# Kernel tuning notes

Measured on AMD Instinct MI355X. Metric: run time of the kernel, lower is better.

The kernel has to match this reference:

```python
import jax, jax.numpy as jnp
import numpy as np

N_NODES = 50000
N_EDGES = 800000
N_GRAPHS = 500
F_NODE = 64
C = 64          # out_channels
F_EDGE = 16     # num_edge_features (== hidden_channels of edge MLP)
N_CLASSES = 2
L = 2           # n_hidden_layers
N_BLOCKS = 6
N_HCONV = N_BLOCKS * L  # 12 hidden PDNConvs
EPS = 1e-5


def setup_inputs() -> dict:
    key = jax.random.key(0)
    ks = jax.random.split(key, 24)

    def w(k, shape, fan_in):
        return (jax.random.normal(k, shape, jnp.float32) / np.sqrt(fan_in)).astype(jnp.float32)

    x = jax.random.normal(ks[0], (N_NODES, F_NODE), jnp.float32)
    src = jax.random.randint(ks[1], (N_EDGES,), 0, N_NODES, dtype=jnp.int32)
    dst = jax.random.randint(ks[2], (N_EDGES,), 0, N_NODES, dtype=jnp.int32)
    edge_index = jnp.stack([src, dst])
    # graph assignment covering all N_GRAPHS segments
    batch = ((jnp.arange(N_NODES) * N_GRAPHS) // N_NODES).astype(jnp.int32)
    edge_attr = jax.random.uniform(ks[3], (N_EDGES, F_EDGE), jnp.float32)

    inp = dict(x=x, edge_index=edge_index, batch=batch, dropout=0, edge_attr=edge_attr)
    # conv1 params
    inp["Wlin1"] = w(ks[4], (F_NODE, C), F_NODE)
    inp["bias1"] = jnp.zeros((C,), jnp.float32)
    inp["m1W1"] = w(ks[5], (F_EDGE, F_EDGE), F_EDGE)
    inp["m1b1"] = jnp.zeros((F_EDGE,), jnp.float32)
    inp["m2W1"] = w(ks[6], (F_EDGE, 1), F_EDGE)
    inp["m2b1"] = jnp.zeros((1,), jnp.float32)
    # 12 stacked hidden PDNConv params
    inp["hWlin"] = w(ks[7], (N_HCONV, C, C), C)
    inp["hbias"] = jnp.zeros((N_HCONV, C), jnp.float32)
    inp["hm1W"] = w(ks[8], (N_HCONV, F_EDGE, F_EDGE), F_EDGE)
    inp["hm1b"] = jnp.zeros((N_HCONV, F_EDGE), jnp.float32)
    inp["hm2W"] = w(ks[9], (N_HCONV, F_EDGE, 1), F_EDGE)
    inp["hm2b"] = jnp.zeros((N_HCONV, 1), jnp.float32)
    # readout linear
    inp["linW"] = w(ks[10], (C, N_CLASSES), C)
    inp["linb"] = jnp.zeros((N_CLASSES,), jnp.float32)
    return inp


def pdn_conv(x, edge_attr, src, dst, mW1, mb1, mW2, mb2, Wlin, bias):
    """PyG PDNConv: edge MLP -> sigmoid edge weight, self-loops, gcn_norm, weighted sum aggregation."""
    n = x.shape[0]
    ew = jax.nn.sigmoid(jax.nn.relu(edge_attr @ mW1 + mb1) @ mW2 + mb2)[:, 0]  # [E]
    loop = jnp.arange(n, dtype=src.dtype)
    s = jnp.concatenate([src, loop])
    d = jnp.concatenate([dst, loop])
    wf = jnp.concatenate([ew, jnp.ones((n,), ew.dtype)])  # self-loop weight = 1
    deg = jax.ops.segment_sum(wf, d, num_segments=n)
    dis = jnp.where(deg > 0, jax.lax.rsqrt(jnp.maximum(deg, 1e-12)), 0.0)
    norm = dis[s] * wf * dis[d]                      # [E+N]
    h = x @ Wlin                                     # [N, C]
    out = jax.ops.segment_sum(h[s] * norm[:, None], d, num_segments=n)
    return out + bias


def bn_relu(x):
    # fresh BatchNorm in training mode: batch stats, weight=1, bias=0 (biased variance)
    mu = x.mean(0)
    var = x.var(0)
    return jax.nn.relu((x - mu) * jax.lax.rsqrt(var + EPS))


def reference(x, edge_index, batch, dropout, edge_attr,
              Wlin1, bias1, m1W1, m1b1, m2W1, m2b1,
              hWlin, hbias, hm1W, hm1b, hm2W, hm2b, linW, linb):
    src, dst = edge_index[0], edge_index[1]
    cur = pdn_conv(x, edge_attr, src, dst, m1W1, m1b1, m2W1, m2b1, Wlin1, bias1)
    xs = [cur]  # dense additive skips: x0, x1, ...
    for b in range(N_BLOCKS):
        for i in range(L):
            j = b * L + i
            cur = pdn_conv(bn_relu(cur), edge_attr, src, dst,
                           hm1W[j], hm1b[j], hm2W[j], hm2b[j], hWlin[j], hbias[j])
        cur = cur + sum(xs)
        xs.append(cur)
    x6 = jax.nn.relu(cur)
    pooled = jax.ops.segment_max(x6, batch, num_segments=N_GRAPHS)  # global max pool
    # dropout is a no-op in eval mode
    return pooled @ linW + linb
```

## Files before the change

### kernel.cpp

```cpp
#include <hip/hip_runtime.h>
#include <math.h>

#define NN 50000
#define NE 800000
#define NG 500
#define NCONV 13
#define WSTRIDE 304
#define SCAN_B 196
#define NBN 12
#define BNP_REPS 64

__device__ __forceinline__ float bl(unsigned u) { return __uint_as_float(u << 16); }
__device__ __forceinline__ float bh(unsigned u) { return __uint_as_float(u & 0xFFFF0000u); }
__device__ __forceinline__ unsigned f2b(float f) {
    unsigned u = __float_as_uint(f);
    return (u + 0x7FFFu + ((u >> 16) & 1u)) >> 16;
}


__global__ void zero_init_k(int* __restrict__ cursor, float* __restrict__ bnpart,
                            const float* __restrict__ m1W1, const float* __restrict__ m1b1,
                            const float* __restrict__ m2W1, const float* __restrict__ m2b1,
                            const float* __restrict__ hm1W, const float* __restrict__ hm1b,
                            const float* __restrict__ hm2W, const float* __restrict__ hm2b,
                            float* __restrict__ wbuf) {
    int i = blockIdx.x * 256 + threadIdx.x;
    if (i < NN) cursor[i] = 0;
    if (i < NBN * BNP_REPS * 128) bnpart[i] = 0.f;
    if (i < NCONV * 289) {
        int cc = i / 289, r = i % 289;
        float v;
        if (r < 256)      v = cc ? hm1W[(cc - 1) * 256 + r] : m1W1[r];
        else if (r < 272) v = cc ? hm1b[(cc - 1) * 16 + (r - 256)] : m1b1[r - 256];
        else if (r < 288) v = cc ? hm2W[(cc - 1) * 16 + (r - 272)] : m2W1[r - 272];
        else              v = cc ? hm2b[cc - 1] : m2b1[0];
        wbuf[cc * WSTRIDE + r] = v;
    }
}


__global__ void count_k(const int* __restrict__ dstp, int* __restrict__ cnt) {
    int e = blockIdx.x * 256 + threadIdx.x;
    if (e >= NE) return;
    atomicAdd(cnt + dstp[e], 1);
}

__global__ __launch_bounds__(256) void scan_blocksum_k(const int* __restrict__ cnt, int* __restrict__ bsum) {
    int i = blockIdx.x * 256 + threadIdx.x;
    int v = (i < NN) ? cnt[i] : 0;
    __shared__ int red[256];
    red[threadIdx.x] = v;
    __syncthreads();
    for (int off = 128; off > 0; off >>= 1) {
        if (threadIdx.x < off) red[threadIdx.x] += red[threadIdx.x + off];
        __syncthreads();
    }
    if (threadIdx.x == 0) bsum[blockIdx.x] = red[0];
}

__global__ __launch_bounds__(256) void scan_bsum_k(int* __restrict__ bsum, int* __restrict__ row_start) {
    __shared__ int ss[256];
    int t = threadIdx.x;
    int v = (t < SCAN_B) ? bsum[t] : 0;
    ss[t] = v;
    __syncthreads();
    for (int off = 1; off < 256; off <<= 1) {
        int add = (t >= off) ? ss[t - off] : 0;
        __syncthreads();
        ss[t] += add;
        __syncthreads();
    }
    if (t < SCAN_B) bsum[t] = (t == 0) ? 0 : ss[t - 1];
    if (t == 0) row_start[NN] = NE;
}

__global__ __launch_bounds__(256) void scan_local_k(int* __restrict__ cnt_cursor, const int* __restrict__ bsum,
                                                    int* __restrict__ row_start) {
    __shared__ int ss[256];
    int i = blockIdx.x * 256 + threadIdx.x;
    int t = threadIdx.x;
    int v = (i < NN) ? cnt_cursor[i] : 0;
    ss[t] = v;
    __syncthreads();
    for (int off = 1; off < 256; off <<= 1) {
        int add = (t >= off) ? ss[t - off] : 0;
        __syncthreads();
        ss[t] += add;
        __syncthreads();
    }
    int excl = bsum[blockIdx.x] + ((t == 0) ? 0 : ss[t - 1]);
    if (i < NN) {
        row_start[i] = excl;
        cnt_cursor[i] = excl;
    }
}

__global__ void scatter_k(const int* __restrict__ srcp, const int* __restrict__ dstp,
                          int* __restrict__ cursor, int* __restrict__ csr_src, int* __restrict__ csr_eid) {
    int e = blockIdx.x * 256 + threadIdx.x;
    if (e >= NE) return;
    int p = atomicAdd(cursor + dstp[e], 1);
    csr_src[p] = srcp[e];
    csr_eid[p] = e;
}


__global__ __launch_bounds__(256, 4) void edge_mlp_k(const float* __restrict__ attr, const int* __restrict__ eid_arr,
                                                     const float* __restrict__ wbuf, float* __restrict__ ew) {
    int k = blockIdx.x * 256 + threadIdx.x;
    if (k >= NE) return;
    int eid = eid_arr[k];
    const float4* a4 = (const float4*)(attr + (size_t)eid * 16);
    float4 A0 = a4[0], A1 = a4[1], A2 = a4[2], A3 = a4[3];
    float a[16] = {A0.x, A0.y, A0.z, A0.w, A1.x, A1.y, A1.z, A1.w,
                   A2.x, A2.y, A2.z, A2.w, A3.x, A3.y, A3.z, A3.w};
    for (int cc = 0; cc < NCONV; cc++) {
        const float* wb = wbuf + cc * WSTRIDE;
        float hb[16];
        #pragma unroll
        for (int o = 0; o < 16; o++) hb[o] = wb[256 + o];
        #pragma unroll
        for (int i = 0; i < 16; i++) {
            float av = a[i];
            #pragma unroll
            for (int o = 0; o < 16; o++) hb[o] = fmaf(av, wb[i * 16 + o], hb[o]);
        }
        float z = wb[288];
        #pragma unroll
        for (int o = 0; o < 16; o++) {
            float hv = hb[o] > 0.f ? hb[o] : 0.f;
            z = fmaf(hv, wb[272 + o], z);
        }
        ew[(size_t)cc * NE + k] = 1.f / (1.f + __expf(-z));
    }
}

__global__ void deg_dis_k(const int* __restrict__ row_start, const float* __restrict__ ew,
                          float* __restrict__ dis) {
    int n = blockIdx.x * 256 + threadIdx.x;
    int cc = blockIdx.y;
    if (n >= NN) return;
    int s0 = row_start[n], s1 = row_start[n + 1];
    const float* e = ew + (size_t)cc * NE;
    float s = 1.f;
    for (int k = s0; k < s1; k++) s += e[k];
    dis[cc * NN + n] = rsqrtf(s);
}


template <bool BN>
__global__ __launch_bounds__(256, 4) void gemm_k(const void* __restrict__ Xv, const float* __restrict__ Wg,
                                                 const float* __restrict__ bnpart, const float* __restrict__ disv,
                                                 unsigned short* __restrict__ Hs) {
    __shared__ float bsum[128];
    __shared__ float mus[64];
    __shared__ float invs[64];
    int t = threadIdx.x;
    if (BN) {
        if (t < 128) {
            float s = 0.f;
            for (int rp = 0; rp < BNP_REPS; rp++) s += bnpart[rp * 128 + t];
            bsum[t] = s;
        }
        __syncthreads();
        if (t < 64) {
            float mu = bsum[t] * (1.f / NN);
            float var = bsum[64 + t] * (1.f / NN) - mu * mu;
            var = var < 0.f ? 0.f : var;
            mus[t] = mu;
            invs[t] = rsqrtf(var + 1e-5f);
        }
        __syncthreads();
    }
    int l = t & 63;
    int colb = __builtin_amdgcn_readfirstlane((t >> 6) * 16);
    int row = blockIdx.x * 64 + l;
    if (row >= NN) return;
    float acc[16];
    #pragma unroll
    for (int c = 0; c < 16; c++) acc[c] = 0.f;
    const float* wcol = Wg + colb;
    if (BN) {
        const uint4* x4 = (const uint4*)((const unsigned short*)Xv + (size_t)row * 64);
        for (int kq = 0; kq < 8; kq++) {
            uint4 uv = x4[kq];
            float xs[8] = {bl(uv.x), bh(uv.x), bl(uv.y), bh(uv.y),
                           bl(uv.z), bh(uv.z), bl(uv.w), bh(uv.w)};
            #pragma unroll
            for (int j = 0; j < 8; j++) {
                int k = kq * 8 + j;
                float v = (xs[j] - mus[k]) * invs[k];
                v = v > 0.f ? v : 0.f;
                const float* wr = wcol + k * 64;
                #pragma unroll
                for (int c = 0; c < 16; c++) acc[c] = fmaf(v, wr[c], acc[c]);
            }
        }
    } else {
        const float4* x4 = (const float4*)((const float*)Xv + (size_t)row * 64);
        for (int kq = 0; kq < 16; kq++) {
            float4 xv = x4[kq];
            float xs[4] = {xv.x, xv.y, xv.z, xv.w};
            #pragma unroll
            for (int j = 0; j < 4; j++) {
                int k = kq * 4 + j;
                float v = xs[j];
                const float* wr = wcol + k * 64;
                #pragma unroll
                for (int c = 0; c < 16; c++) acc[c] = fmaf(v, wr[c], acc[c]);
            }
        }
    }
    float dsc = disv[row];
    unsigned out[8];
    #pragma unroll
    for (int q = 0; q < 8; q++) {
        out[q] = f2b(acc[2 * q] * dsc) | (f2b(acc[2 * q + 1] * dsc) << 16);
    }
    uint4* o4 = (uint4*)(Hs + (size_t)row * 64 + colb);
    uint4 t0; t0.x = out[0]; t0.y = out[1]; t0.z = out[2]; t0.w = out[3];
    uint4 t1; t1.x = out[4]; t1.y = out[5]; t1.z = out[6]; t1.w = out[7];
    o4[0] = t0;
    o4[1] = t1;
}


template <int MODE, int STATS>
__global__ __launch_bounds__(256) void aggregate_k(const unsigned short* __restrict__ Hs, const int* __restrict__ row_start,
                                                   const int* __restrict__ csr_src, const float* __restrict__ w,
                                                   const float* __restrict__ dis, const float* __restrict__ bias,
                                                   unsigned short* __restrict__ curb16, float* __restrict__ S,
                                                   float* __restrict__ finalv, float* __restrict__ bnpart) {
    int t = threadIdx.x;
    int wvid = t >> 6;
    int lane = t & 63;
    int g = lane >> 3;
    int li = lane & 7;
    int node = blockIdx.x * 32 + wvid * 8 + g;
    bool valid = node < NN;
    int s0 = 0, s1 = 0;
    if (valid) { s0 = row_start[node]; s1 = row_start[node + 1]; }
    int fb = li * 8;
    size_t oi = (size_t)node * 64 + fb;
    float dn = 0.f;
    uint4 us = {0, 0, 0, 0};
    float4 b0 = {0, 0, 0, 0}, b1 = {0, 0, 0, 0};
    float4 sa = {0, 0, 0, 0}, sb = {0, 0, 0, 0};
    if (valid) {
        dn = dis[node];
        us = *(const uint4*)(Hs + (size_t)node * 64 + fb);
        b0 = *(const float4*)(bias + fb);
        b1 = *(const float4*)(bias + fb + 4);
        if (MODE >= 2) {
            sa = *(const float4*)(S + oi);
            sb = *(const float4*)(S + oi + 4);
        }
    }
    float acc[8];
    #pragma unroll
    for (int j = 0; j < 8; j++) acc[j] = 0.f;
    int k = s0;
    for (; k + 4 <= s1; k += 4) {
        int i0 = csr_src[k], i1 = csr_src[k + 1], i2 = csr_src[k + 2], i3 = csr_src[k + 3];
        float w0 = w[k], w1 = w[k + 1], w2 = w[k + 2], w3 = w[k + 3];
        uint4 u0 = *(const uint4*)(Hs + (size_t)i0 * 64 + fb);
        uint4 u1 = *(const uint4*)(Hs + (size_t)i1 * 64 + fb);
        uint4 u2 = *(const uint4*)(Hs + (size_t)i2 * 64 + fb);
        uint4 u3 = *(const uint4*)(Hs + (size_t)i3 * 64 + fb);
        acc[0] = fmaf(bl(u0.x), w0, acc[0]); acc[1] = fmaf(bh(u0.x), w0, acc[1]);
        acc[2] = fmaf(bl(u0.y), w0, acc[2]); acc[3] = fmaf(bh(u0.y), w0, acc[3]);
        acc[4] = fmaf(bl(u0.z), w0, acc[4]); acc[5] = fmaf(bh(u0.z), w0, acc[5]);
        acc[6] = fmaf(bl(u0.w), w0, acc[6]); acc[7] = fmaf(bh(u0.w), w0, acc[7]);
        acc[0] = fmaf(bl(u1.x), w1, acc[0]); acc[1] = fmaf(bh(u1.x), w1, acc[1]);
        acc[2] = fmaf(bl(u1.y), w1, acc[2]); acc[3] = fmaf(bh(u1.y), w1, acc[3]);
        acc[4] = fmaf(bl(u1.z), w1, acc[4]); acc[5] = fmaf(bh(u1.z), w1, acc[5]);
        acc[6] = fmaf(bl(u1.w), w1, acc[6]); acc[7] = fmaf(bh(u1.w), w1, acc[7]);
        acc[0] = fmaf(bl(u2.x), w2, acc[0]); acc[1] = fmaf(bh(u2.x), w2, acc[1]);
        acc[2] = fmaf(bl(u2.y), w2, acc[2]); acc[3] = fmaf(bh(u2.y), w2, acc[3]);
        acc[4] = fmaf(bl(u2.z), w2, acc[4]); acc[5] = fmaf(bh(u2.z), w2, acc[5]);
        acc[6] = fmaf(bl(u2.w), w2, acc[6]); acc[7] = fmaf(bh(u2.w), w2, acc[7]);
        acc[0] = fmaf(bl(u3.x), w3, acc[0]); acc[1] = fmaf(bh(u3.x), w3, acc[1]);
        acc[2] = fmaf(bl(u3.y), w3, acc[2]); acc[3] = fmaf(bh(u3.y), w3, acc[3]);
        acc[4] = fmaf(bl(u3.z), w3, acc[4]); acc[5] = fmaf(bh(u3.z), w3, acc[5]);
        acc[6] = fmaf(bl(u3.w), w3, acc[6]); acc[7] = fmaf(bh(u3.w), w3, acc[7]);
    }
    for (; k < s1; k++) {
        int ia = csr_src[k];
        float wa = w[k];
        uint4 ua = *(const uint4*)(Hs + (size_t)ia * 64 + fb);
        acc[0] = fmaf(bl(ua.x), wa, acc[0]); acc[1] = fmaf(bh(ua.x), wa, acc[1]);
        acc[2] = fmaf(bl(ua.y), wa, acc[2]); acc[3] = fmaf(bh(ua.y), wa, acc[3]);
        acc[4] = fmaf(bl(ua.z), wa, acc[4]); acc[5] = fmaf(bh(ua.z), wa, acc[5]);
        acc[6] = fmaf(bl(ua.w), wa, acc[6]); acc[7] = fmaf(bh(ua.w), wa, acc[7]);
    }
    float vv[8];
    #pragma unroll
    for (int j = 0; j < 8; j++) vv[j] = 0.f;
    if (valid) {
        float hs[8] = {bl(us.x), bh(us.x), bl(us.y), bh(us.y), bl(us.z), bh(us.z), bl(us.w), bh(us.w)};
        float bb[8] = {b0.x, b0.y, b0.z, b0.w, b1.x, b1.y, b1.z, b1.w};
        #pragma unroll
        for (int j = 0; j < 8; j++) vv[j] = fmaf(dn, acc[j] + hs[j], bb[j]);
        if (MODE >= 2) {
            float ss[8] = {sa.x, sa.y, sa.z, sa.w, sb.x, sb.y, sb.z, sb.w};
            #pragma unroll
            for (int j = 0; j < 8; j++) vv[j] += ss[j];
            if (MODE == 2) {
                *(float4*)(S + oi) = make_float4(ss[0] + vv[0], ss[1] + vv[1], ss[2] + vv[2], ss[3] + vv[3]);
                *(float4*)(S + oi + 4) = make_float4(ss[4] + vv[4], ss[5] + vv[5], ss[6] + vv[6], ss[7] + vv[7]);
            }
        }
        if (MODE == 1) {
            *(float4*)(S + oi) = make_float4(vv[0], vv[1], vv[2], vv[3]);
            *(float4*)(S + oi + 4) = make_float4(vv[4], vv[5], vv[6], vv[7]);
        }
        if (MODE == 3) {
            *(float4*)(finalv + oi) = make_float4(vv[0], vv[1], vv[2], vv[3]);
            *(float4*)(finalv + oi + 4) = make_float4(vv[4], vv[5], vv[6], vv[7]);
        } else {
            uint4 ob;
            ob.x = f2b(vv[0]) | (f2b(vv[1]) << 16);
            ob.y = f2b(vv[2]) | (f2b(vv[3]) << 16);
            ob.z = f2b(vv[4]) | (f2b(vv[5]) << 16);
            ob.w = f2b(vv[6]) | (f2b(vv[7]) << 16);
            *(uint4*)(curb16 + oi) = ob;
        }
    }
    if (STATS) {
        __shared__ float reds[32 * 65];
        __shared__ float redq[32 * 65];
        int gg = wvid * 8 + g;
        #pragma unroll
        for (int j = 0; j < 8; j++) {
            float v = valid ? vv[j] : 0.f;
            reds[gg * 65 + fb + j] = v;
            redq[gg * 65 + fb + j] = v * v;
        }
        __syncthreads();
        if (t < 128) {
            int f = t & 63;
            const float* src = (t < 64) ? reds : redq;
            float s = 0.f;
            #pragma unroll
            for (int i = 0; i < 32; i++) s += src[i * 65 + f];
            int rep = blockIdx.x & (BNP_REPS - 1);
            atomicAdd(bnpart + rep * 128 + ((t < 64) ? 0 : 64) + f, s);
        }
    }
}


__global__ __launch_bounds__(256) void pool_final_k(const float* __restrict__ cur, const float* __restrict__ linW,
                                                    const float* __restrict__ linb, float* __restrict__ outp) {
    int gph = blockIdx.x;
    int c = threadIdx.x & 63, rq = threadIdx.x >> 6;
    int r0 = gph * 100;
    float m = 0.f;
    for (int r = r0 + rq; r < r0 + 100; r += 4) {
        float v = cur[(size_t)r * 64 + c];
        m = v > m ? v : m;
    }
    __shared__ float red[256];
    red[threadIdx.x] = m;
    __syncthreads();
    if (rq == 0) {
        float a = red[c], b = red[64 + c], d = red[128 + c], e = red[192 + c];
        a = a > b ? a : b;
        d = d > e ? d : e;
        a = a > d ? a : d;
        float p0 = a * linW[c * 2 + 0];
        float p1 = a * linW[c * 2 + 1];
        #pragma unroll
        for (int off = 32; off > 0; off >>= 1) {
            p0 += __shfl_down(p0, off, 64);
            p1 += __shfl_down(p1, off, 64);
        }
        if (c == 0) {
            outp[gph * 2 + 0] = p0 + linb[0];
            outp[gph * 2 + 1] = p1 + linb[1];
        }
    }
}


extern "C" void kernel_launch(void* const* d_in, const int* in_sizes, int n_in,
                              void* d_out, int out_size, void* d_ws, size_t ws_size,
                              hipStream_t stream) {
    const float* x        = (const float*)d_in[0];
    const int*   ei       = (const int*)d_in[1];
    const int*   srcp     = ei;
    const int*   dstp     = ei + NE;
    const float* edge_attr= (const float*)d_in[4];
    const float* Wlin1    = (const float*)d_in[5];
    const float* bias1    = (const float*)d_in[6];
    const float* m1W1     = (const float*)d_in[7];
    const float* m1b1     = (const float*)d_in[8];
    const float* m2W1     = (const float*)d_in[9];
    const float* m2b1     = (const float*)d_in[10];
    const float* hWlin    = (const float*)d_in[11];
    const float* hbias    = (const float*)d_in[12];
    const float* hm1W     = (const float*)d_in[13];
    const float* hm1b     = (const float*)d_in[14];
    const float* hm2W     = (const float*)d_in[15];
    const float* hm2b     = (const float*)d_in[16];
    const float* linW     = (const float*)d_in[17];
    const float* linb     = (const float*)d_in[18];
    float* outp = (float*)d_out;

    char* ws = (char*)d_ws;
    size_t off = 0;
    auto alloc = [&](size_t bytes) -> char* {
        char* p = ws + off;
        off += (bytes + 255) & ~(size_t)255;
        return p;
    };
    int*   cursor   = (int*)alloc((size_t)NN * 4);
    int*   row_start= (int*)alloc((size_t)(NN + 1) * 4);
    int*   csr_src  = (int*)alloc((size_t)NE * 4);
    int*   csr_eid  = (int*)alloc((size_t)NE * 4);
    float* ewbuf    = (float*)alloc((size_t)NCONV * NE * 4);
    float* disbuf   = (float*)alloc((size_t)NCONV * NN * 4);
    unsigned short* hbuf   = (unsigned short*)alloc((size_t)NN * 64 * 2);
    unsigned short* curb16 = (unsigned short*)alloc((size_t)NN * 64 * 2);
    float* Sbuf     = (float*)alloc((size_t)NN * 64 * 4);
    float* finalbuf = (float*)alloc((size_t)NN * 64 * 4);
    float* bnpart   = (float*)alloc((size_t)NBN * BNP_REPS * 128 * 4);
    float* wbuf     = (float*)alloc((size_t)NCONV * WSTRIDE * 4);
    int*   bsum     = (int*)alloc((size_t)SCAN_B * 4);

    const int TB = 256;
    int gN   = (NN + TB - 1) / TB;
    int gE   = (NE + TB - 1) / TB;
    int gA   = (NN + 31) / 32;
    int gB   = (NN + 63) / 64;
    int gZ   = (NBN * BNP_REPS * 128) / TB;

    zero_init_k<<<gZ, TB, 0, stream>>>(cursor, bnpart, m1W1, m1b1, m2W1, m2b1, hm1W, hm1b, hm2W, hm2b, wbuf);
    count_k<<<gE, TB, 0, stream>>>(dstp, cursor);
    scan_blocksum_k<<<SCAN_B, TB, 0, stream>>>(cursor, bsum);
    scan_bsum_k<<<1, TB, 0, stream>>>(bsum, row_start);
    scan_local_k<<<SCAN_B, TB, 0, stream>>>(cursor, bsum, row_start);
    scatter_k<<<gE, TB, 0, stream>>>(srcp, dstp, cursor, csr_src, csr_eid);

    edge_mlp_k<<<gE, TB, 0, stream>>>(edge_attr, csr_eid, wbuf, ewbuf);
    deg_dis_k<<<dim3(gN, NCONV), TB, 0, stream>>>(row_start, ewbuf, disbuf);

    for (int cj = 0; cj < NCONV; cj++) {
        const float* Win  = (cj == 0) ? Wlin1 : (hWlin + (size_t)(cj - 1) * 4096);
        const float* bin  = (cj == 0) ? bias1 : (hbias + (size_t)(cj - 1) * 64);
        const float* dcc  = disbuf + (size_t)cj * NN;
        if (cj > 0) {
            gemm_k<true><<<gB, TB, 0, stream>>>(curb16, Win, bnpart + (size_t)(cj - 1) * BNP_REPS * 128, dcc, hbuf);
        } else {
            gemm_k<false><<<gB, TB, 0, stream>>>(x, Win, nullptr, dcc, hbuf);
        }
        const float* wcc = ewbuf + (size_t)cj * NE;
        float* bnp = (cj < NBN) ? (bnpart + (size_t)cj * BNP_REPS * 128) : nullptr;
        if (cj == 0)
            aggregate_k<1, 1><<<gA, TB, 0, stream>>>(hbuf, row_start, csr_src, wcc, dcc, bin, curb16, Sbuf, finalbuf, bnp);
        else if (cj == 12)
            aggregate_k<3, 0><<<gA, TB, 0, stream>>>(hbuf, row_start, csr_src, wcc, dcc, bin, curb16, Sbuf, finalbuf, bnp);
        else if ((cj & 1) == 0)
            aggregate_k<2, 1><<<gA, TB, 0, stream>>>(hbuf, row_start, csr_src, wcc, dcc, bin, curb16, Sbuf, finalbuf, bnp);
        else
            aggregate_k<0, 1><<<gA, TB, 0, stream>>>(hbuf, row_start, csr_src, wcc, dcc, bin, curb16, Sbuf, finalbuf, bnp);
    }

    pool_final_k<<<NG, TB, 0, stream>>>(finalbuf, linW, linb, outp);
}
```

Baseline: 861.6 us.

## Sort aggregation nodes by in-degree and deepen gather unroll

Builds a degree histogram and counting-sort permutation of nodes once, then has each aggregate kernel process nodes in degree-sorted order so the 8 nodes sharing a wavefront have similar edge counts, reducing divergence and idle lanes. The inner gather loop is also unrolled to 8 outstanding loads with a 2-wide remainder to raise memory-level parallelism. The cost is three small extra setup kernels, an extra perm lookup per node, and output writes that become scattered rather than contiguous across neighbouring nodes.

```diff
diff --git a/kernel.cpp b/kernel.cpp
--- a/kernel.cpp
+++ b/kernel.cpp
@@ -19,6 +19,7 @@
 
 
 __global__ void zero_init_k(int* __restrict__ cursor, float* __restrict__ bnpart,
+                            int* __restrict__ hist,
                             const float* __restrict__ m1W1, const float* __restrict__ m1b1,
                             const float* __restrict__ m2W1, const float* __restrict__ m2b1,
                             const float* __restrict__ hm1W, const float* __restrict__ hm1b,
@@ -27,6 +28,7 @@
     int i = blockIdx.x * 256 + threadIdx.x;
     if (i < NN) cursor[i] = 0;
     if (i < NBN * BNP_REPS * 128) bnpart[i] = 0.f;
+    if (i < 256) hist[i] = 0;
     if (i < NCONV * 289) {
         int cc = i / 289, r = i % 289;
         float v;
@@ -102,6 +104,39 @@
     int p = atomicAdd(cursor + dstp[e], 1);
     csr_src[p] = srcp[e];
     csr_eid[p] = e;
+}
+
+
+__global__ void deg_hist_k(const int* __restrict__ row_start, int* __restrict__ hist) {
+    int n = blockIdx.x * 256 + threadIdx.x;
+    if (n >= NN) return;
+    int d = row_start[n + 1] - row_start[n];
+    if (d > 255) d = 255;
+    atomicAdd(hist + d, 1);
+}
+
+__global__ __launch_bounds__(256) void hist_scan_k(int* __restrict__ hist) {
+    __shared__ int ss[256];
+    int t = threadIdx.x;
+    ss[t] = hist[t];
+    __syncthreads();
+    for (int off = 1; off < 256; off <<= 1) {
+        int add = (t >= off) ? ss[t - off] : 0;
+        __syncthreads();
+        ss[t] += add;
+        __syncthreads();
+    }
+    hist[t] = (t == 0) ? 0 : ss[t - 1];
+}
+
+__global__ void perm_scatter_k(const int* __restrict__ row_start, int* __restrict__ hist,
+                               int* __restrict__ perm) {
+    int n = blockIdx.x * 256 + threadIdx.x;
+    if (n >= NN) return;
+    int d = row_start[n + 1] - row_start[n];
+    if (d > 255) d = 255;
+    int p = atomicAdd(hist + d, 1);
+    perm[p] = n;
 }
 
 
@@ -227,6 +262,7 @@
 
 template <int MODE, int STATS>
 __global__ __launch_bounds__(256) void aggregate_k(const unsigned short* __restrict__ Hs, const int* __restrict__ row_start,
+                                                   const int* __restrict__ perm,
                                                    const int* __restrict__ csr_src, const float* __restrict__ w,
                                                    const float* __restrict__ dis, const float* __restrict__ bias,
                                                    unsigned short* __restrict__ curb16, float* __restrict__ S,
@@ -236,10 +272,15 @@
     int lane = t & 63;
     int g = lane >> 3;
     int li = lane & 7;
-    int node = blockIdx.x * 32 + wvid * 8 + g;
-    bool valid = node < NN;
+    int idx = blockIdx.x * 32 + wvid * 8 + g;
+    bool valid = idx < NN;
+    int node = 0;
     int s0 = 0, s1 = 0;
-    if (valid) { s0 = row_start[node]; s1 = row_start[node + 1]; }
+    if (valid) {
+        node = perm[idx];
+        s0 = row_start[node];
+        s1 = row_start[node + 1];
+    }
     int fb = li * 8;
     size_t oi = (size_t)node * 64 + fb;
     float dn = 0.f;
@@ -260,31 +301,38 @@
     #pragma unroll
     for (int j = 0; j < 8; j++) acc[j] = 0.f;
     int k = s0;
-    for (; k + 4 <= s1; k += 4) {
-        int i0 = csr_src[k], i1 = csr_src[k + 1], i2 = csr_src[k + 2], i3 = csr_src[k + 3];
-        float w0 = w[k], w1 = w[k + 1], w2 = w[k + 2], w3 = w[k + 3];
-        uint4 u0 = *(const uint4*)(Hs + (size_t)i0 * 64 + fb);
-        uint4 u1 = *(const uint4*)(Hs + (size_t)i1 * 64 + fb);
-        uint4 u2 = *(const uint4*)(Hs + (size_t)i2 * 64 + fb);
-        uint4 u3 = *(const uint4*)(Hs + (size_t)i3 * 64 + fb);
-        acc[0] = fmaf(bl(u0.x), w0, acc[0]); acc[1] = fmaf(bh(u0.x), w0, acc[1]);
-        acc[2] = fmaf(bl(u0.y), w0, acc[2]); acc[3] = fmaf(bh(u0.y), w0, acc[3]);
-        acc[4] = fmaf(bl(u0.z), w0, acc[4]); acc[5] = fmaf(bh(u0.z), w0, acc[5]);
-        acc[6] = fmaf(bl(u0.w), w0, acc[6]); acc[7] = fmaf(bh(u0.w), w0, acc[7]);
-        acc[0] = fmaf(bl(u1.x), w1, acc[0]); acc[1] = fmaf(bh(u1.x), w1, acc[1]);
-        acc[2] = fmaf(bl(u1.y), w1, acc[2]); acc[3] = fmaf(bh(u1.y), w1, acc[3]);
-        acc[4] = fmaf(bl(u1.z), w1, acc[4]); acc[5] = fmaf(bh(u1.z), w1, acc[5]);
-        acc[6] = fmaf(bl(u1.w), w1, acc[6]); acc[7] = fmaf(bh(u1.w), w1, acc[7]);
-        acc[0] = fmaf(bl(u2.x), w2, acc[0]); acc[1] = fmaf(bh(u2.x), w2, acc[1]);
-        acc[2] = fmaf(bl(u2.y), w2, acc[2]); acc[3] = fmaf(bh(u2.y), w2, acc[3]);
-        acc[4] = fmaf(bl(u2.z), w2, acc[4]); acc[5] = fmaf(bh(u2.z), w2, acc[5]);
-        acc[6] = fmaf(bl(u2.w), w2, acc[6]); acc[7] = fmaf(bh(u2.w), w2, acc[7]);
-        acc[0] = fmaf(bl(u3.x), w3, acc[0]); acc[1] = fmaf(bh(u3.x), w3, acc[1]);
-        acc[2] = fmaf(bl(u3.y), w3, acc[2]); acc[3] = fmaf(bh(u3.y), w3, acc[3]);
-        acc[4] = fmaf(bl(u3.z), w3, acc[4]); acc[5] = fmaf(bh(u3.z), w3, acc[5]);
-        acc[6] = fmaf(bl(u3.w), w3, acc[6]); acc[7] = fmaf(bh(u3.w), w3, acc[7]);
-    }
-    for (; k < s1; k++) {
+    for (; k + 8 <= s1; k += 8) {
+        int ii[8];
+        float ww[8];
+        uint4 uu[8];
+        #pragma unroll
+        for (int q = 0; q < 8; q++) { ii[q] = csr_src[k + q]; ww[q] = w[k + q]; }
+        #pragma unroll
+        for (int q = 0; q < 8; q++) uu[q] = *(const uint4*)(Hs + (size_t)ii[q] * 64 + fb);
+        #pragma unroll
+        for (int q = 0; q < 8; q++) {
+            float wq = ww[q];
+            acc[0] = fmaf(bl(uu[q].x), wq, acc[0]); acc[1] = fmaf(bh(uu[q].x), wq, acc[1]);
+            acc[2] = fmaf(bl(uu[q].y), wq, acc[2]); acc[3] = fmaf(bh(uu[q].y), wq, acc[3]);
+            acc[4] = fmaf(bl(uu[q].z), wq, acc[4]); acc[5] = fmaf(bh(uu[q].z), wq, acc[5]);
+            acc[6] = fmaf(bl(uu[q].w), wq, acc[6]); acc[7] = fmaf(bh(uu[q].w), wq, acc[7]);
+        }
+    }
+    for (; k + 2 <= s1; k += 2) {
+        int ia = csr_src[k], ib = csr_src[k + 1];
+        float wa = w[k], wb = w[k + 1];
+        uint4 ua = *(const uint4*)(Hs + (size_t)ia * 64 + fb);
+        uint4 ub = *(const uint4*)(Hs + (size_t)ib * 64 + fb);
+        acc[0] = fmaf(bl(ua.x), wa, acc[0]); acc[1] = fmaf(bh(ua.x), wa, acc[1]);
+        acc[2] = fmaf(bl(ua.y), wa, acc[2]); acc[3] = fmaf(bh(ua.y), wa, acc[3]);
+        acc[4] = fmaf(bl(ua.z), wa, acc[4]); acc[5] = fmaf(bh(ua.z), wa, acc[5]);
+        acc[6] = fmaf(bl(ua.w), wa, acc[6]); acc[7] = fmaf(bh(ua.w), wa, acc[7]);
+        acc[0] = fmaf(bl(ub.x), wb, acc[0]); acc[1] = fmaf(bh(ub.x), wb, acc[1]);
+        acc[2] = fmaf(bl(ub.y), wb, acc[2]); acc[3] = fmaf(bh(ub.y), wb, acc[3]);
+        acc[4] = fmaf(bl(ub.z), wb, acc[4]); acc[5] = fmaf(bh(ub.z), wb, acc[5]);
+        acc[6] = fmaf(bl(ub.w), wb, acc[6]); acc[7] = fmaf(bh(ub.w), wb, acc[7]);
+    }
+    if (k < s1) {
         int ia = csr_src[k];
         float wa = w[k];
         uint4 ua = *(const uint4*)(Hs + (size_t)ia * 64 + fb);
@@ -427,6 +475,8 @@
     float* bnpart   = (float*)alloc((size_t)NBN * BNP_REPS * 128 * 4);
     float* wbuf     = (float*)alloc((size_t)NCONV * WSTRIDE * 4);
     int*   bsum     = (int*)alloc((size_t)SCAN_B * 4);
+    int*   hist     = (int*)alloc(256 * 4);
+    int*   perm     = (int*)alloc((size_t)NN * 4);
 
     const int TB = 256;
     int gN   = (NN + TB - 1) / TB;
@@ -435,12 +485,16 @@
     int gB   = (NN + 63) / 64;
     int gZ   = (NBN * BNP_REPS * 128) / TB;
 
-    zero_init_k<<<gZ, TB, 0, stream>>>(cursor, bnpart, m1W1, m1b1, m2W1, m2b1, hm1W, hm1b, hm2W, hm2b, wbuf);
+    zero_init_k<<<gZ, TB, 0, stream>>>(cursor, bnpart, hist, m1W1, m1b1, m2W1, m2b1, hm1W, hm1b, hm2W, hm2b, wbuf);
     count_k<<<gE, TB, 0, stream>>>(dstp, cursor);
     scan_blocksum_k<<<SCAN_B, TB, 0, stream>>>(cursor, bsum);
     scan_bsum_k<<<1, TB, 0, stream>>>(bsum, row_start);
     scan_local_k<<<SCAN_B, TB, 0, stream>>>(cursor, bsum, row_start);
     scatter_k<<<gE, TB, 0, stream>>>(srcp, dstp, cursor, csr_src, csr_eid);
+
+    deg_hist_k<<<gN, TB, 0, stream>>>(row_start, hist);
+    hist_scan_k<<<1, TB, 0, stream>>>(hist);
+    perm_scatter_k<<<gN, TB, 0, stream>>>(row_start, hist, perm);
 
     edge_mlp_k<<<gE, TB, 0, stream>>>(edge_attr, csr_eid, wbuf, ewbuf);
     deg_dis_k<<<dim3(gN, NCONV), TB, 0, stream>>>(row_start, ewbuf, disbuf);
@@ -457,13 +511,13 @@
         const float* wcc = ewbuf + (size_t)cj * NE;
         float* bnp = (cj < NBN) ? (bnpart + (size_t)cj * BNP_REPS * 128) : nullptr;
         if (cj == 0)
-            aggregate_k<1, 1><<<gA, TB, 0, stream>>>(hbuf, row_start, csr_src, wcc, dcc, bin, curb16, Sbuf, finalbuf, bnp);
+            aggregate_k<1, 1><<<gA, TB, 0, stream>>>(hbuf, row_start, perm, csr_src, wcc, dcc, bin, curb16, Sbuf, finalbuf, bnp);
         else if (cj == 12)
-            aggregate_k<3, 0><<<gA, TB, 0, stream>>>(hbuf, row_start, csr_src, wcc, dcc, bin, curb16, Sbuf, finalbuf, bnp);
+            aggregate_k<3, 0><<<gA, TB, 0, stream>>>(hbuf, row_start, perm, csr_src, wcc, dcc, bin, curb16, Sbuf, finalbuf, bnp);
         else if ((cj & 1) == 0)
-            aggregate_k<2, 1><<<gA, TB, 0, stream>>>(hbuf, row_start, csr_src, wcc, dcc, bin, curb16, Sbuf, finalbuf, bnp);
+            aggregate_k<2, 1><<<gA, TB, 0, stream>>>(hbuf, row_start, perm, csr_src, wcc, dcc, bin, curb16, Sbuf, finalbuf, bnp);
         else
-            aggregate_k<0, 1><<<gA, TB, 0, stream>>>(hbuf, row_start, csr_src, wcc, dcc, bin, curb16, Sbuf, finalbuf, bnp);
+            aggregate_k<0, 1><<<gA, TB, 0, stream>>>(hbuf, row_start, perm, csr_src, wcc, dcc, bin, curb16, Sbuf, finalbuf, bnp);
     }
 
     pool_final_k<<<NG, TB, 0, stream>>>(finalbuf, linW, linb, outp);
```

Result: slower. 1.129 ms (+31.0%).
